# Optimization experiments

Measured on AMD Instinct MI355X. Metric: run time of the kernel, lower is better.

The kernel has to match this reference:

```python
import jax, jax.numpy as jnp
import numpy as np

D_MODEL = 1024
D_STATE = 128
D_CONV = 4
EXPAND = 2
HEADDIM = 64
D_INNER = EXPAND * D_MODEL            # 2048
NHEADS = D_INNER // HEADDIM           # 32
CONV_DIM = D_INNER + 2 * D_STATE      # 2304 (x, B, C share the conv)
D_IN_PROJ = 2 * D_INNER + 2 * D_STATE + NHEADS  # 4384 (z, xBC, dt)
CHUNK = 64
BATCH, SEQ = 8, 2048
EPS = 1e-5


def setup_inputs() -> dict:
    key = jax.random.key(0)
    ks = jax.random.split(key, 8)
    x = jax.random.normal(ks[0], (BATCH, SEQ, D_MODEL), dtype=jnp.float32)
    ln_w = jnp.ones((D_MODEL,), jnp.float32)
    ln_b = jnp.zeros((D_MODEL,), jnp.float32)
    W_in = jax.random.normal(ks[1], (D_IN_PROJ, D_MODEL), jnp.float32) * 0.02
    conv_w = jax.random.normal(ks[2], (CONV_DIM, D_CONV), jnp.float32) * 0.2
    conv_b = jnp.zeros((CONV_DIM,), jnp.float32)
    # dt_bias ~ inverse-softplus of dt in [1e-3, 1e-1]
    dt = jnp.exp(jax.random.uniform(ks[3], (NHEADS,), jnp.float32,
                                    minval=float(np.log(1e-3)), maxval=float(np.log(1e-1))))
    dt_bias = dt + jnp.log(-jnp.expm1(-dt))
    A_log = jnp.log(jax.random.uniform(ks[4], (NHEADS,), jnp.float32, minval=1.0, maxval=16.0))
    D = jnp.ones((NHEADS,), jnp.float32)
    rms_w = jnp.ones((D_INNER,), jnp.float32)
    W_out = jax.random.normal(ks[5], (D_MODEL, D_INNER), jnp.float32) * 0.02
    return {"x": x, "ln_w": ln_w, "ln_b": ln_b, "W_in": W_in, "conv_w": conv_w,
            "conv_b": conv_b, "dt_bias": dt_bias, "A_log": A_log, "D": D,
            "rms_w": rms_w, "W_out": W_out}


def _segsum(a):
    # a: (..., T) -> (..., T, T) cumulative segment sums, -inf above diagonal
    T = a.shape[-1]
    cs = jnp.cumsum(a, axis=-1)
    d = cs[..., :, None] - cs[..., None, :]
    return jnp.where(jnp.tril(jnp.ones((T, T), bool)), d, -jnp.inf)


def _mamba2_layer(x, ln_w, ln_b, W_in, conv_w, conv_b, dt_bias, A_log, D, rms_w, W_out):
    b, l, _ = x.shape
    # LayerNorm
    mu = jnp.mean(x, -1, keepdims=True)
    xc = x - mu
    var = jnp.mean(xc * xc, -1, keepdims=True)
    xn = xc * jax.lax.rsqrt(var + EPS) * ln_w + ln_b
    # in_proj -> z, xBC, dt
    zxbcdt = xn @ W_in.T                                  # (b,l,D_IN_PROJ)
    z = zxbcdt[..., :D_INNER]
    xBC = zxbcdt[..., D_INNER:D_INNER + CONV_DIM]
    dt = zxbcdt[..., D_INNER + CONV_DIM:]
    dt = jax.nn.softplus(dt + dt_bias)                    # (b,l,h)
    # causal depthwise conv1d (kernel D_CONV) + SiLU
    xp = jnp.pad(xBC, ((0, 0), (D_CONV - 1, 0), (0, 0)))
    conv = conv_b + sum(xp[:, k:k + l, :] * conv_w[:, k] for k in range(D_CONV))
    xBC = conv * jax.nn.sigmoid(conv)
    xs = xBC[..., :D_INNER].reshape(b, l, NHEADS, HEADDIM)          # (b,l,h,p)
    Bm = xBC[..., D_INNER:D_INNER + D_STATE]                         # (b,l,n) ngroups=1
    Cm = xBC[..., D_INNER + D_STATE:]                                # (b,l,n)
    # SSD chunked scan
    A = -jnp.exp(A_log)                                              # (h,)
    A_dt = dt * A                                                    # (b,l,h)
    Xdt = xs * dt[..., None]                                         # (b,l,h,p)
    nc = l // CHUNK
    Xc = Xdt.reshape(b, nc, CHUNK, NHEADS, HEADDIM)                  # (b,c,s,h,p)
    Ac = A_dt.reshape(b, nc, CHUNK, NHEADS).transpose(0, 3, 1, 2)    # (b,h,c,s)
    Bc = Bm.reshape(b, nc, CHUNK, D_STATE)                           # (b,c,s,n)
    Cc = Cm.reshape(b, nc, CHUNK, D_STATE)
    A_cs = jnp.cumsum(Ac, -1)                                        # (b,h,c,s)
    Lmat = jnp.exp(_segsum(Ac))                                      # (b,h,c,s,s)
    Y_diag = jnp.einsum('bcln,bcsn,bhcls,bcshp->bclhp', Cc, Bc, Lmat, Xc)
    decay_states = jnp.exp(A_cs[..., -1:] - A_cs)                    # (b,h,c,s)
    states = jnp.einsum('bcln,bhcl,bclhp->bchpn', Bc, decay_states, Xc)
    states = jnp.concatenate([jnp.zeros_like(states[:, :1]), states], axis=1)
    chunk_sum = jnp.pad(A_cs[..., -1], ((0, 0), (0, 0), (1, 0)))     # (b,h,c+1)
    decay_chunk = jnp.exp(_segsum(chunk_sum))                        # (b,h,c+1,c+1)
    new_states = jnp.einsum('bhzc,bchpn->bzhpn', decay_chunk, states)
    states_prev = new_states[:, :-1]                                 # (b,c,h,p,n)
    state_decay_out = jnp.exp(A_cs)                                  # (b,h,c,s)
    Y_off = jnp.einsum('bcln,bchpn,bhcl->bclhp', Cc, states_prev, state_decay_out)
    Y = (Y_diag + Y_off).reshape(b, l, NHEADS, HEADDIM)
    Y = Y + xs * D[None, None, :, None]
    y = Y.reshape(b, l, D_INNER)
    # gated RMSNorm: gate first, then normalize
    y = y * (z * jax.nn.sigmoid(z))
    y = y * jax.lax.rsqrt(jnp.mean(y * y, -1, keepdims=True) + EPS) * rms_w
    out = y @ W_out.T
    return x + out


def reference(x, ln_w, ln_b, W_in, conv_w, conv_b, dt_bias, A_log, D, rms_w, W_out):
    return _mamba2_layer(x, ln_w, ln_b, W_in, conv_w, conv_b, dt_bias, A_log, D, rms_w, W_out)
```

## Files before the change

### kernel.cpp

```cpp
#include <hip/hip_runtime.h>
#include <hip/hip_bf16.h>
#include <math.h>

typedef __hip_bfloat16 bf16;
typedef short short8 __attribute__((ext_vector_type(8)));
typedef short short4v __attribute__((ext_vector_type(4)));
typedef float f32x4 __attribute__((ext_vector_type(4)));

#define B_ 8
#define L_ 2048
#define DM 1024
#define DI 2048
#define NH 32
#define HD 64
#define DS 128
#define NWPAD 4480
#define XW 2432
#define CONVD 2304
#define NC 32
#define CK 64
#define HG 16
#define NGRP (NH / HG)
#define BL (B_ * L_)

static __device__ __forceinline__ f32x4 mfma_bf16(short8 a, short8 b, f32x4 c) {
  asm("v_mfma_f32_16x16x32_bf16 %0, %1, %2, %0" : "+v"(c) : "v"(a), "v"(b));
  return c;
}

static __device__ __forceinline__ void gload16(const bf16* g, bf16* l) {
  __builtin_amdgcn_global_load_lds((const __attribute__((address_space(1))) void*)g,
                                   (__attribute__((address_space(3))) void*)l, 16, 0, 0);
}

static __device__ __forceinline__ short bf2s(float f) {
  bf16 b = __float2bfloat16(f);
  return *reinterpret_cast<short*>(&b);
}

static __device__ __forceinline__ float s2f(short s) {
  unsigned int u = ((unsigned int)(unsigned short)s) << 16;
  return __uint_as_float(u);
}

__global__ void cvt_k(const float* __restrict__ Wi, const float* __restrict__ Wo,
                      bf16* __restrict__ Wib, bf16* __restrict__ Wob) {
  size_t i = (size_t)blockIdx.x * 256 + threadIdx.x;
  const size_t NWI = (size_t)NWPAD * DM;
  if (i < NWI) {
    float v = (i < (size_t)4384 * 1024) ? Wi[i] : 0.f;
    Wib[i] = __float2bfloat16(v);
  } else {
    size_t j = i - NWI;
    Wob[j] = __float2bfloat16(Wo[j]);
  }
}

__global__ void ln_k(const float* __restrict__ x, const float* __restrict__ w,
                     const float* __restrict__ bz, bf16* __restrict__ xn) {
  __shared__ float sm1[4], sm2[4];
  int row = blockIdx.x, tid = threadIdx.x;
  int d0 = tid * 4;
  const float* xr = x + (size_t)row * DM;
  float4 v4 = *(const float4*)&xr[d0];
  float v[4] = {v4.x, v4.y, v4.z, v4.w};
  float s = v[0] + v[1] + v[2] + v[3];
#pragma unroll
  for (int o = 32; o > 0; o >>= 1) s += __shfl_down(s, o, 64);
  if ((tid & 63) == 0) sm1[tid >> 6] = s;
  __syncthreads();
  float mean = (sm1[0] + sm1[1] + sm1[2] + sm1[3]) * (1.f / DM);
  float q = 0.f;
#pragma unroll
  for (int i = 0; i < 4; i++) { float d = v[i] - mean; q += d * d; }
#pragma unroll
  for (int o = 32; o > 0; o >>= 1) q += __shfl_down(q, o, 64);
  if ((tid & 63) == 0) sm2[tid >> 6] = q;
  __syncthreads();
  float rstd = rsqrtf((sm2[0] + sm2[1] + sm2[2] + sm2[3]) * (1.f / DM) + 1e-5f);
  float4 w4 = *(const float4*)&w[d0];
  float4 b4 = *(const float4*)&bz[d0];
  short4v o4;
  o4[0] = bf2s((v[0] - mean) * rstd * w4.x + b4.x);
  o4[1] = bf2s((v[1] - mean) * rstd * w4.y + b4.y);
  o4[2] = bf2s((v[2] - mean) * rstd * w4.z + b4.z);
  o4[3] = bf2s((v[3] - mean) * rstd * w4.w + b4.w);
  *(short4v*)&xn[(size_t)row * DM + d0] = o4;
}

#define GEMM_PROLOGUE(Kdim)                                                     \
  const int tid = threadIdx.x;                                                  \
  const int lane = tid & 63;                                                    \
  const int wave = tid >> 6;                                                    \
  int nwg = gridDim.x * gridDim.y;                                              \
  int id = blockIdx.y * gridDim.x + blockIdx.x;                                 \
  int bx = blockIdx.x, by = blockIdx.y;                                         \
  if ((nwg & 7) == 0) {                                                         \
    int swz = (id & 7) * (nwg >> 3) + (id >> 3);                                \
    bx = swz % gridDim.x;                                                       \
    by = swz / gridDim.x;                                                       \
  }                                                                             \
  const int m0 = by * 128, n0 = bx * 128;                                       \
  const int wm = (wave >> 1) * 64, wn = (wave & 1) * 64;                        \
  const int srow = tid >> 3;                                                    \
  const int schunk = tid & 7;                                                   \
  f32x4 acc[4][4];                                                              \
  _Pragma("unroll")                                                             \
  for (int i = 0; i < 4; i++)                                                   \
    _Pragma("unroll")                                                           \
    for (int j = 0; j < 4; j++) acc[i][j] = (f32x4){0.f, 0.f, 0.f, 0.f};        \
  for (int kt = 0; kt < (Kdim); kt += 64) {                                     \
    __syncthreads();                                                            \
    _Pragma("unroll")                                                           \
    for (int is = 0; is < 4; is++) {                                            \
      int row = is * 32 + srow;                                                 \
      int gcol = (schunk ^ (row & 7)) << 3;                                     \
      const bf16* ga = A + (size_t)(m0 + row) * (Kdim) + kt + gcol;             \
      const bf16* gb = Bw + (size_t)(n0 + row) * (Kdim) + kt + gcol;            \
      bf16* la = &As[(is * 32 + wave * 8) * 64];                                \
      bf16* lb = &Bs[(is * 32 + wave * 8) * 64];                                \
      gload16(ga, la);                                                          \
      gload16(gb, lb);                                                          \
    }                                                                           \
    __syncthreads();                                                            \
    _Pragma("unroll")                                                           \
    for (int kk = 0; kk < 2; kk++) {                                            \
      short8 af[4], bfr[4];                                                     \
      int mrow = lane & 15;                                                     \
      int kch = kk * 4 + (lane >> 4);                                           \
      _Pragma("unroll")                                                         \
      for (int mi = 0; mi < 4; mi++) {                                          \
        int r = wm + mi * 16 + mrow;                                            \
        af[mi] = *(const short8*)&As[r * 64 + ((kch ^ (r & 7)) << 3)];          \
      }                                                                         \
      _Pragma("unroll")                                                         \
      for (int ni = 0; ni < 4; ni++) {                                          \
        int r = wn + ni * 16 + mrow;                                            \
        bfr[ni] = *(const short8*)&Bs[r * 64 + ((kch ^ (r & 7)) << 3)];         \
      }                                                                         \
      _Pragma("unroll")                                                         \
      for (int mi = 0; mi < 4; mi++)                                            \
        _Pragma("unroll")                                                       \
        for (int ni = 0; ni < 4; ni++)                                          \
          acc[mi][ni] = mfma_bf16(af[mi], bfr[ni], acc[mi][ni]);                \
    }                                                                           \
  }                                                                             \
  asm volatile("s_nop 7\n\ts_nop 7" ::);                                        \
  const int orow = (lane >> 4) << 2;                                            \
  const int ocol = lane & 15;

__global__ __launch_bounds__(256) void gemm_inproj_k(
    const bf16* __restrict__ A, const bf16* __restrict__ Bw,
    bf16* __restrict__ zb, bf16* __restrict__ xb) {
  __shared__ bf16 As[128 * 64];
  __shared__ bf16 Bs[128 * 64];
  GEMM_PROLOGUE(DM)
#pragma unroll
  for (int mi = 0; mi < 4; mi++) {
#pragma unroll
    for (int ni = 0; ni < 4; ni++) {
      int rbase = m0 + wm + mi * 16 + orow;
      int cc = n0 + wn + ni * 16 + ocol;
#pragma unroll
      for (int r = 0; r < 4; r++) {
        bf16 v = __float2bfloat16(acc[mi][ni][r]);
        if (cc < DI) zb[(size_t)(rbase + r) * DI + cc] = v;
        else         xb[(size_t)(rbase + r) * XW + (cc - DI)] = v;
      }
    }
  }
}

__global__ __launch_bounds__(256) void gemm_out_k(
    const bf16* __restrict__ A, const bf16* __restrict__ Bw,
    float* __restrict__ C, const float* __restrict__ resid) {
  __shared__ bf16 As[128 * 64];
  __shared__ bf16 Bs[128 * 64];
  GEMM_PROLOGUE(DI)
#pragma unroll
  for (int mi = 0; mi < 4; mi++) {
#pragma unroll
    for (int ni = 0; ni < 4; ni++) {
      int rbase = m0 + wm + mi * 16 + orow;
      int cc = n0 + wn + ni * 16 + ocol;
#pragma unroll
      for (int r = 0; r < 4; r++) {
        size_t idx = (size_t)(rbase + r) * DM + cc;
        C[idx] = acc[mi][ni][r] + resid[idx];
      }
    }
  }
}

__global__ void conv_k(const bf16* __restrict__ xbc, const float* __restrict__ conv_w,
                       const float* __restrict__ conv_b, bf16* __restrict__ xsb,
                       bf16* __restrict__ Bb, bf16* __restrict__ Cb) {
  int c = blockIdx.x * 256 + threadIdx.x;
  int lbase = blockIdx.y * 16;
  int b = blockIdx.z;
  float4 w = ((const float4*)conv_w)[c];
  float bias = conv_b[c];
  const bf16* xp = xbc + (size_t)b * L_ * XW + c;
  float h0 = 0.f, h1 = 0.f, h2 = 0.f;
  if (lbase > 0) {
    h0 = __bfloat162float(xp[(size_t)(lbase - 3) * XW]);
    h1 = __bfloat162float(xp[(size_t)(lbase - 2) * XW]);
    h2 = __bfloat162float(xp[(size_t)(lbase - 1) * XW]);
  }
  for (int t = 0; t < 16; t++) {
    int l = lbase + t;
    float x3 = __bfloat162float(xp[(size_t)l * XW]);
    float v = bias + w.x * h0 + w.y * h1 + w.z * h2 + w.w * x3;
    v = v / (1.f + __expf(-v));
    bf16 o = __float2bfloat16(v);
    size_t rl = (size_t)b * L_ + l;
    if (c < DI)           xsb[rl * DI + c] = o;
    else if (c < DI + DS) Bb[rl * DS + (c - DI)] = o;
    else                  Cb[rl * DS + (c - DI - DS)] = o;
    h0 = h1; h1 = h2; h2 = x3;
  }
}

__global__ void dt_k(const bf16* __restrict__ xbc, const float* __restrict__ dt_bias,
                     const float* __restrict__ A_log, float* __restrict__ dtsp,
                     float* __restrict__ dta) {
  size_t i = (size_t)blockIdx.x * 256 + threadIdx.x;
  int h = (int)(i >> 14);
  size_t row = i & 16383;
  float raw = __bfloat162float(xbc[row * XW + CONVD + h]) + dt_bias[h];
  float sp = (raw > 20.f) ? raw : log1pf(__expf(raw));
  dtsp[i] = sp;
  dta[i] = -__expf(A_log[h]) * sp;
}

__global__ __launch_bounds__(256) void chunk_g_k(
    const bf16* __restrict__ xsb, const bf16* __restrict__ Bb, const bf16* __restrict__ Cb,
    const float* __restrict__ dtsp, const float* __restrict__ dta,
    const float* __restrict__ Dv, int hbase,
    bf16* __restrict__ Y, bf16* __restrict__ states, float* __restrict__ cs63) {
  __shared__ __align__(16) bf16 Bs[64][136];
  __shared__ __align__(16) bf16 Cs[64][136];
  __shared__ __align__(16) bf16 Btw[128][72];
  __shared__ __align__(16) bf16 Xt[64][72];
  __shared__ __align__(16) bf16 Sb[64][72];
  __shared__ float cs[64];
  __shared__ float wts[64];
  __shared__ float dts[64];

  int hgsub = blockIdx.x, c = blockIdx.y, b = blockIdx.z;
  int tid = threadIdx.x;
  int lane = tid & 63, wid = tid >> 6;
  size_t l0 = (size_t)b * L_ + (size_t)c * CK;

  for (int i = tid; i < 64 * 16; i += 256) {
    int r = i >> 4, n8 = (i & 15) << 3;
    *(short8*)&Bs[r][n8] = *(const short8*)&Bb[(l0 + r) * DS + n8];
    *(short8*)&Cs[r][n8] = *(const short8*)&Cb[(l0 + r) * DS + n8];
  }
  __syncthreads();

  f32x4 accg[4];
#pragma unroll
  for (int i = 0; i < 4; i++) accg[i] = (f32x4){0.f, 0.f, 0.f, 0.f};
  {
    int rb = wid * 16 + (lane & 15);
    int c0 = (lane >> 4) * 8;
#pragma unroll
    for (int kk = 0; kk < 4; kk++) {
      int kc = c0 + kk * 32;
      short8 bfrag = *(const short8*)&Bs[rb][kc];
#pragma unroll
      for (int lt = 0; lt < 4; lt++) {
        short8 afrag = *(const short8*)&Cs[lt * 16 + (lane & 15)][kc];
        accg[lt] = mfma_bf16(afrag, bfrag, accg[lt]);
      }
    }
  }
  asm volatile("s_nop 7\n\ts_nop 7" ::);

  for (int hh = 0; hh < 8; hh++) {
    int hl = hgsub * 8 + hh;
    int h = hbase + hl;
    __syncthreads();

    {
      const bf16* xp = xsb + l0 * DI + h * HD + lane;
      for (int oct = wid; oct < 8; oct += 4) {
        int lb = oct * 8;
        short8 v;
#pragma unroll
        for (int j = 0; j < 8; j++)
          v[j] = *(const short*)&xp[(size_t)(lb + j) * DI];
        *(short8*)&Xt[lane][lb] = v;
      }
    }
    if (tid < 64) {
      dts[tid] = dtsp[(size_t)h * BL + l0 + tid];
      wts[tid] = dta[(size_t)h * BL + l0 + tid];
    }
    __syncthreads();
    if (tid < 64) {
      float a = wts[tid];
#pragma unroll
      for (int o = 1; o < 64; o <<= 1) {
        float t = __shfl_up(a, o, 64);
        if (lane >= o) a += t;
      }
      cs[tid] = a;
      float tot = __shfl(a, 63, 64);
      if (tid == 63) cs63[((size_t)b * NH + h) * NC + c] = a;
      wts[tid] = __expf(tot - a) * dts[tid];
    }
    __syncthreads();

    for (int u = wid; u < 16; u += 4) {
      int nh = u & 1, oct = u >> 1;
      int n = nh * 64 + lane;
      int lb = oct * 8;
      short8 v;
#pragma unroll
      for (int j = 0; j < 8; j++)
        v[j] = bf2s(__bfloat162float(Bs[lb + j][n]) * wts[lb + j]);
      *(short8*)&Btw[n][lb] = v;
    }
    {
      int s = wid * 16 + (lane & 15);
      float css = cs[s], dtss = dts[s];
#pragma unroll
      for (int lt = 0; lt < 4; lt++) {
#pragma unroll
        for (int r = 0; r < 4; r++) {
          int l = lt * 16 + ((lane >> 4) << 2) + r;
          float v = (s <= l) ? accg[lt][r] * __expf(cs[l] - css) * dtss : 0.f;
          Sb[l][s] = __float2bfloat16(v);
        }
      }
    }
    __syncthreads();

    f32x4 accy[4];
#pragma unroll
    for (int i = 0; i < 4; i++) accy[i] = (f32x4){0.f, 0.f, 0.f, 0.f};
    {
      int prow = wid * 16 + (lane & 15);
      int c0 = (lane >> 4) * 8;
#pragma unroll
      for (int kk = 0; kk < 2; kk++) {
        int kc = c0 + kk * 32;
        short8 xfrag = *(const short8*)&Xt[prow][kc];
#pragma unroll
        for (int lt = 0; lt < 4; lt++) {
          short8 sfrag = *(const short8*)&Sb[lt * 16 + (lane & 15)][kc];
          accy[lt] = mfma_bf16(sfrag, xfrag, accy[lt]);
        }
      }
    }
    f32x4 accs[4][2];
#pragma unroll
    for (int i = 0; i < 4; i++)
#pragma unroll
      for (int j = 0; j < 2; j++) accs[i][j] = (f32x4){0.f, 0.f, 0.f, 0.f};
    {
      int c0 = (lane >> 4) * 8;
#pragma unroll
      for (int kk = 0; kk < 2; kk++) {
        int kc = c0 + kk * 32;
        short8 bf0 = *(const short8*)&Btw[wid * 32 + (lane & 15)][kc];
        short8 bf1 = *(const short8*)&Btw[wid * 32 + 16 + (lane & 15)][kc];
#pragma unroll
        for (int pt = 0; pt < 4; pt++) {
          short8 xfrag = *(const short8*)&Xt[pt * 16 + (lane & 15)][kc];
          accs[pt][0] = mfma_bf16(xfrag, bf0, accs[pt][0]);
          accs[pt][1] = mfma_bf16(xfrag, bf1, accs[pt][1]);
        }
      }
    }
    asm volatile("s_nop 7\n\ts_nop 7" ::);
    {
      float Dh = Dv[h];
      int p = wid * 16 + (lane & 15);
#pragma unroll
      for (int lt = 0; lt < 4; lt++) {
#pragma unroll
        for (int r = 0; r < 4; r++) {
          int l = lt * 16 + ((lane >> 4) << 2) + r;
          float xv = __bfloat162float(Xt[p][l]);
          Y[(l0 + l) * DI + h * HD + p] = __float2bfloat16(accy[lt][r] + Dh * xv);
        }
      }
    }
    {
      size_t sbb = ((((size_t)b * NC + c) * HG + hl) * HD) * DS;
#pragma unroll
      for (int pt = 0; pt < 4; pt++)
#pragma unroll
        for (int tn = 0; tn < 2; tn++)
#pragma unroll
          for (int r = 0; r < 4; r++) {
            int p = pt * 16 + ((lane >> 4) << 2) + r;
            int n = wid * 32 + tn * 16 + (lane & 15);
            states[sbb + (size_t)p * DS + n] = __float2bfloat16(accs[pt][tn][r]);
          }
    }
  }
}

__global__ void scan_k(bf16* __restrict__ states, const float* __restrict__ cs63,
                       int hbase) {
  int hl = blockIdx.x, b = blockIdx.y, sp = blockIdx.z;
  int tid = threadIdx.x;
  const float* csb = cs63 + ((size_t)b * NH + hbase + hl) * NC;
  int e0 = sp * 1024 + tid * 4;
  float S0 = 0.f, S1 = 0.f, S2 = 0.f, S3 = 0.f;
  for (int c = 0; c < NC; c++) {
    bf16* p = states + ((((size_t)b * NC + c) * HG + hl) * HD) * DS + e0;
    float d = __expf(csb[c]);
    short4v cur = *(const short4v*)p;
    short4v prev;
    prev[0] = bf2s(S0); prev[1] = bf2s(S1); prev[2] = bf2s(S2); prev[3] = bf2s(S3);
    *(short4v*)p = prev;
    S0 = S0 * d + s2f(cur[0]);
    S1 = S1 * d + s2f(cur[1]);
    S2 = S2 * d + s2f(cur[2]);
    S3 = S3 * d + s2f(cur[3]);
  }
}

__global__ __launch_bounds__(256) void yoff_k(
    const bf16* __restrict__ Cb, const bf16* __restrict__ states,
    const float* __restrict__ dta, int hbase, bf16* __restrict__ Y) {
  __shared__ __align__(16) bf16 Cs[64][136];
  __shared__ __align__(16) bf16 Sp[64][136];
  __shared__ float cs[64];
  int hl = blockIdx.x, c = blockIdx.y, b = blockIdx.z;
  int h = hbase + hl;
  int tid = threadIdx.x;
  int lane = tid & 63, wid = tid >> 6;
  size_t l0 = (size_t)b * L_ + (size_t)c * CK;
  for (int i = tid; i < 64 * 16; i += 256) {
    int r = i >> 4, n8 = (i & 15) << 3;
    *(short8*)&Cs[r][n8] = *(const short8*)&Cb[(l0 + r) * DS + n8];
  }
  size_t sbb = ((((size_t)b * NC + c) * HG + hl) * HD) * DS;
  for (int i = tid; i < 64 * 16; i += 256) {
    int p = i >> 4, n8 = (i & 15) << 3;
    *(short8*)&Sp[p][n8] = *(const short8*)&states[sbb + (size_t)p * DS + n8];
  }
  if (tid < 64) cs[tid] = dta[(size_t)h * BL + l0 + tid];
  __syncthreads();
  if (tid < 64) {
    float a = cs[tid];
#pragma unroll
    for (int o = 1; o < 64; o <<= 1) {
      float t = __shfl_up(a, o, 64);
      if (lane >= o) a += t;
    }
    cs[tid] = a;
  }
  __syncthreads();
  f32x4 acc[4];
#pragma unroll
  for (int i = 0; i < 4; i++) acc[i] = (f32x4){0.f, 0.f, 0.f, 0.f};
  {
    int prow = wid * 16 + (lane & 15);
    int c0 = (lane >> 4) * 8;
#pragma unroll
    for (int kk = 0; kk < 4; kk++) {
      int kc = c0 + kk * 32;
      short8 sfrag = *(const short8*)&Sp[prow][kc];
#pragma unroll
      for (int lt = 0; lt < 4; lt++) {
        short8 cfrag = *(const short8*)&Cs[lt * 16 + (lane & 15)][kc];
        acc[lt] = mfma_bf16(cfrag, sfrag, acc[lt]);
      }
    }
  }
  asm volatile("s_nop 7\n\ts_nop 7" ::);
  {
    int p = wid * 16 + (lane & 15);
#pragma unroll
    for (int lt = 0; lt < 4; lt++) {
#pragma unroll
      for (int r = 0; r < 4; r++) {
        int l = lt * 16 + ((lane >> 4) << 2) + r;
        float e = __expf(cs[l]);
        size_t idx = (l0 + l) * DI + h * HD + p;
        Y[idx] = __float2bfloat16(__bfloat162float(Y[idx]) + e * acc[lt][r]);
      }
    }
  }
}

__global__ void gate_k(const bf16* __restrict__ Y, const bf16* __restrict__ z,
                       const float* __restrict__ rms_w, bf16* __restrict__ yb) {
  __shared__ float sm[4];
  int row = blockIdx.x, tid = threadIdx.x;
  int d0 = tid * 8;
  const bf16* Yr = Y + (size_t)row * DI;
  const bf16* zr = z + (size_t)row * DI;
  short8 yv8 = *(const short8*)&Yr[d0];
  short8 zv8 = *(const short8*)&zr[d0];
  float v[8]; float ss = 0.f;
#pragma unroll
  for (int i = 0; i < 8; i++) {
    float yv = s2f(yv8[i]);
    float zz = s2f(zv8[i]);
    yv *= zz / (1.f + __expf(-zz));
    v[i] = yv; ss += yv * yv;
  }
#pragma unroll
  for (int o = 32; o > 0; o >>= 1) ss += __shfl_down(ss, o, 64);
  if ((tid & 63) == 0) sm[tid >> 6] = ss;
  __syncthreads();
  float rstd = rsqrtf((sm[0] + sm[1] + sm[2] + sm[3]) * (1.f / DI) + 1e-5f);
  short8 o8;
#pragma unroll
  for (int i = 0; i < 8; i++) o8[i] = bf2s(v[i] * rstd * rms_w[d0 + i]);
  *(short8*)&yb[(size_t)row * DI + d0] = o8;
}

extern "C" void kernel_launch(void* const* d_in, const int* in_sizes, int n_in,
                              void* d_out, int out_size, void* d_ws, size_t ws_size,
                              hipStream_t stream) {
  const float* x       = (const float*)d_in[0];
  const float* ln_w    = (const float*)d_in[1];
  const float* ln_b    = (const float*)d_in[2];
  const float* W_in    = (const float*)d_in[3];
  const float* conv_w  = (const float*)d_in[4];
  const float* conv_b  = (const float*)d_in[5];
  const float* dt_bias = (const float*)d_in[6];
  const float* A_log   = (const float*)d_in[7];
  const float* Dv      = (const float*)d_in[8];
  const float* rms_w   = (const float*)d_in[9];
  const float* W_out   = (const float*)d_in[10];
  float* out = (float*)d_out;

  char* ws = (char*)d_ws;
  size_t off = 0;
  auto alloc = [&](size_t bytes) -> void* {
    void* p = ws + off;
    off += (bytes + 255) & ~(size_t)255;
    return p;
  };
  bf16*  W_in_b  = (bf16*)alloc((size_t)NWPAD * DM * 2);
  bf16*  W_out_b = (bf16*)alloc((size_t)DM * DI * 2);
  bf16*  R1      = (bf16*)alloc((size_t)BL * XW * 2);
  bf16*  R2      = (bf16*)alloc((size_t)BL * DI * 2);
  bf16*  Bb      = (bf16*)alloc((size_t)BL * DS * 2);
  bf16*  Cb      = (bf16*)alloc((size_t)BL * DS * 2);
  float* dtsp    = (float*)alloc((size_t)BL * NH * 4);
  float* dta     = (float*)alloc((size_t)BL * NH * 4);
  float* cs63    = (float*)alloc((size_t)B_ * NH * NC * 4);
  bf16* xbcdt  = R1;
  bf16* states = R1;
  bf16* yb     = R1;
  bf16* xn     = R2;
  bf16* xsb    = R2;
  bf16* zbuf   = (bf16*)d_out;
  (void)ws_size; (void)in_sizes; (void)n_in; (void)out_size;

  cvt_k <<<(NWPAD * DM + DM * DI) / 256, 256, 0, stream>>>(W_in, W_out, W_in_b, W_out_b);
  ln_k  <<<BL, 256, 0, stream>>>(x, ln_w, ln_b, xn);
  gemm_inproj_k<<<dim3(NWPAD / 128, BL / 128), 256, 0, stream>>>(
      xn, W_in_b, zbuf, xbcdt);
  conv_k<<<dim3(CONVD / 256, L_ / 16, B_), 256, 0, stream>>>(
      xbcdt, conv_w, conv_b, xsb, Bb, Cb);
  dt_k  <<<(BL * NH) / 256, 256, 0, stream>>>(xbcdt, dt_bias, A_log, dtsp, dta);
  for (int g = 0; g < NGRP; g++) {
    int hbase = g * HG;
    chunk_g_k<<<dim3(2, NC, B_), 256, 0, stream>>>(xsb, Bb, Cb, dtsp, dta, Dv, hbase,
                                                   xsb , states, cs63);
    scan_k   <<<dim3(HG, B_, 8), 256, 0, stream>>>(states, cs63, hbase);
    yoff_k   <<<dim3(HG, NC, B_), 256, 0, stream>>>(Cb, states, dta, hbase, xsb );
  }
  gate_k<<<BL, 256, 0, stream>>>(xsb , zbuf, rms_w, yb);
  gemm_out_k<<<dim3(DM / 128, BL / 128), 256, 0, stream>>>(yb, W_out_b, out, x);
}
```

Baseline: 569.7 us.

## Rewrite GEMMs as 256x256 double-buffered pipelined tiles with 8 waves

```diff
diff --git a/kernel.cpp b/kernel.cpp
--- a/kernel.cpp
+++ b/kernel.cpp
@@ -14,7 +14,7 @@
 #define NH 32
 #define HD 64
 #define DS 128
-#define NWPAD 4480
+#define NWPAD 4608
 #define XW 2432
 #define CONVD 2304
 #define NC 32
@@ -88,7 +88,76 @@
   *(short4v*)&xn[(size_t)row * DM + d0] = o4;
 }
 
-#define GEMM_PROLOGUE(Kdim)                                                     \
+static __device__ __forceinline__ void stage_half(const bf16* __restrict__ gbase, int Kd,
+                                                  bf16* lbase, int H, int kti,
+                                                  int srow, int schunk, int wave) {
+  int gc = (schunk ^ (srow & 7)) << 3;
+  const bf16* g = gbase + (size_t)(H * 128 + srow) * Kd + (size_t)kti * 64 + gc;
+  bf16* l = lbase + (H * 128 + wave * 8) * 64;
+  gload16(g, l);
+  gload16(g + (size_t)64 * Kd, l + 64 * 64);
+}
+
+#define BARM asm volatile("s_barrier" ::: "memory")
+
+#define RD_A(mi)                                                                \
+  {                                                                             \
+    int r = wm + (mi) * 16 + (lane & 15);                                       \
+    int k0 = lane >> 4;                                                         \
+    af[mi][0] = *(const short8*)&Asb[r * 64 + ((k0 ^ (r & 7)) << 3)];           \
+    af[mi][1] = *(const short8*)&Asb[r * 64 + (((k0 + 4) ^ (r & 7)) << 3)];     \
+  }
+#define RD_B(ni)                                                                \
+  {                                                                             \
+    int r = wn + (ni) * 16 + (lane & 15);                                       \
+    int k0 = lane >> 4;                                                         \
+    bfr[ni][0] = *(const short8*)&Bsb[r * 64 + ((k0 ^ (r & 7)) << 3)];          \
+    bfr[ni][1] = *(const short8*)&Bsb[r * 64 + (((k0 + 4) ^ (r & 7)) << 3)];    \
+  }
+#define MFMA_Q(q)                                                               \
+  __builtin_amdgcn_s_setprio(1);                                                \
+  _Pragma("unroll") for (int ni = 0; ni < 4; ni++)                              \
+    acc[2*(q)][ni] = mfma_bf16(af[2*(q)][0], bfr[ni][0], acc[2*(q)][ni]);       \
+  _Pragma("unroll") for (int ni = 0; ni < 4; ni++)                              \
+    acc[2*(q)+1][ni] = mfma_bf16(af[2*(q)+1][0], bfr[ni][0], acc[2*(q)+1][ni]); \
+  _Pragma("unroll") for (int ni = 0; ni < 4; ni++)                              \
+    acc[2*(q)][ni] = mfma_bf16(af[2*(q)][1], bfr[ni][1], acc[2*(q)][ni]);       \
+  _Pragma("unroll") for (int ni = 0; ni < 4; ni++)                              \
+    acc[2*(q)+1][ni] = mfma_bf16(af[2*(q)+1][1], bfr[ni][1], acc[2*(q)+1][ni]); \
+  __builtin_amdgcn_s_setprio(0);
+
+#define TILE4(b, t, Kd)                                                         \
+  {                                                                             \
+    const bf16* Asb = &As[b][0];                                                \
+    const bf16* Bsb = &Bs[b][0];                                                \
+    const int i1 = ((t) + 1 < NKT) ? (t) + 1 : NKT - 1;                         \
+    const int i2 = ((t) + 2 < NKT) ? (t) + 2 : NKT - 1;                         \
+    RD_B(0) RD_B(1) RD_B(2) RD_B(3)                                             \
+    RD_A(0) RD_A(1)                                                             \
+    stage_half(Ag, Kd, &As[(b) ^ 1][0], 1, i1, srow, schunk, wave);             \
+    asm volatile("s_waitcnt lgkmcnt(8)" ::: "memory");                          \
+    BARM;                                                                       \
+    MFMA_Q(0)                                                                   \
+    BARM;                                                                       \
+    RD_A(2) RD_A(3) RD_A(4) RD_A(5)                                             \
+    stage_half(Bg, Kd, &Bs[b][0], 0, i2, srow, schunk, wave);                   \
+    BARM;                                                                       \
+    MFMA_Q(1)                                                                   \
+    BARM;                                                                       \
+    RD_A(6) RD_A(7)                                                             \
+    stage_half(Bg, Kd, &Bs[b][0], 1, i2, srow, schunk, wave);                   \
+    asm volatile("s_waitcnt lgkmcnt(0)" ::: "memory");                          \
+    BARM;                                                                       \
+    MFMA_Q(2)                                                                   \
+    BARM;                                                                       \
+    stage_half(Ag, Kd, &As[b][0], 0, i2, srow, schunk, wave);                   \
+    asm volatile("s_waitcnt vmcnt(6)" ::: "memory");                            \
+    BARM;                                                                       \
+    MFMA_Q(3)                                                                   \
+    BARM;                                                                       \
+  }
+
+#define GEMM8_BODY(Kd)                                                          \
   const int tid = threadIdx.x;                                                  \
   const int lane = tid & 63;                                                    \
   const int wave = tid >> 6;                                                    \
@@ -100,63 +169,44 @@
     bx = swz % gridDim.x;                                                       \
     by = swz / gridDim.x;                                                       \
   }                                                                             \
-  const int m0 = by * 128, n0 = bx * 128;                                       \
-  const int wm = (wave >> 1) * 64, wn = (wave & 1) * 64;                        \
-  const int srow = tid >> 3;                                                    \
-  const int schunk = tid & 7;                                                   \
-  f32x4 acc[4][4];                                                              \
-  _Pragma("unroll")                                                             \
-  for (int i = 0; i < 4; i++)                                                   \
-    _Pragma("unroll")                                                           \
-    for (int j = 0; j < 4; j++) acc[i][j] = (f32x4){0.f, 0.f, 0.f, 0.f};        \
-  for (int kt = 0; kt < (Kdim); kt += 64) {                                     \
-    __syncthreads();                                                            \
-    _Pragma("unroll")                                                           \
-    for (int is = 0; is < 4; is++) {                                            \
-      int row = is * 32 + srow;                                                 \
-      int gcol = (schunk ^ (row & 7)) << 3;                                     \
-      const bf16* ga = A + (size_t)(m0 + row) * (Kdim) + kt + gcol;             \
-      const bf16* gb = Bw + (size_t)(n0 + row) * (Kdim) + kt + gcol;            \
-      bf16* la = &As[(is * 32 + wave * 8) * 64];                                \
-      bf16* lb = &Bs[(is * 32 + wave * 8) * 64];                                \
-      gload16(ga, la);                                                          \
-      gload16(gb, lb);                                                          \
-    }                                                                           \
-    __syncthreads();                                                            \
-    _Pragma("unroll")                                                           \
-    for (int kk = 0; kk < 2; kk++) {                                            \
-      short8 af[4], bfr[4];                                                     \
-      int mrow = lane & 15;                                                     \
-      int kch = kk * 4 + (lane >> 4);                                           \
-      _Pragma("unroll")                                                         \
-      for (int mi = 0; mi < 4; mi++) {                                          \
-        int r = wm + mi * 16 + mrow;                                            \
-        af[mi] = *(const short8*)&As[r * 64 + ((kch ^ (r & 7)) << 3)];          \
-      }                                                                         \
-      _Pragma("unroll")                                                         \
-      for (int ni = 0; ni < 4; ni++) {                                          \
-        int r = wn + ni * 16 + mrow;                                            \
-        bfr[ni] = *(const short8*)&Bs[r * 64 + ((kch ^ (r & 7)) << 3)];         \
-      }                                                                         \
-      _Pragma("unroll")                                                         \
-      for (int mi = 0; mi < 4; mi++)                                            \
-        _Pragma("unroll")                                                       \
-        for (int ni = 0; ni < 4; ni++)                                          \
-          acc[mi][ni] = mfma_bf16(af[mi], bfr[ni], acc[mi][ni]);                \
-    }                                                                           \
+  const int m0 = by * 256, n0 = bx * 256;                                       \
+  const int wm = (wave >> 2) * 128, wn = (wave & 3) * 64;                       \
+  const int srow = tid >> 3, schunk = tid & 7;                                  \
+  const bf16* Ag = A + (size_t)m0 * (Kd);                                       \
+  const bf16* Bg = Bw + (size_t)n0 * (Kd);                                      \
+  const int NKT = (Kd) / 64;                                                    \
+  f32x4 acc[8][4];                                                              \
+  short8 af[8][2], bfr[4][2];                                                   \
+  _Pragma("unroll") for (int i = 0; i < 8; i++)                                 \
+    _Pragma("unroll") for (int j = 0; j < 4; j++)                               \
+      acc[i][j] = (f32x4){0.f, 0.f, 0.f, 0.f};                                  \
+  stage_half(Bg, Kd, &Bs[0][0], 0, 0, srow, schunk, wave);                      \
+  stage_half(Bg, Kd, &Bs[0][0], 1, 0, srow, schunk, wave);                      \
+  stage_half(Ag, Kd, &As[0][0], 0, 0, srow, schunk, wave);                      \
+  stage_half(Ag, Kd, &As[0][0], 1, 0, srow, schunk, wave);                      \
+  asm volatile("s_waitcnt vmcnt(4)" ::: "memory");                              \
+  stage_half(Bg, Kd, &Bs[1][0], 0, 1, srow, schunk, wave);                      \
+  stage_half(Bg, Kd, &Bs[1][0], 1, 1, srow, schunk, wave);                      \
+  stage_half(Ag, Kd, &As[1][0], 0, 1, srow, schunk, wave);                      \
+  asm volatile("s_waitcnt vmcnt(6)" ::: "memory");                              \
+  BARM;                                                                         \
+  for (int t = 0; t < NKT; t += 2) {                                            \
+    TILE4(0, t, Kd)                                                             \
+    TILE4(1, t + 1, Kd)                                                         \
   }                                                                             \
+  asm volatile("s_waitcnt vmcnt(0)" ::: "memory");                              \
   asm volatile("s_nop 7\n\ts_nop 7" ::);                                        \
   const int orow = (lane >> 4) << 2;                                            \
   const int ocol = lane & 15;
 
-__global__ __launch_bounds__(256) void gemm_inproj_k(
+__global__ __launch_bounds__(512, 2) void gemm_inproj_k(
     const bf16* __restrict__ A, const bf16* __restrict__ Bw,
     bf16* __restrict__ zb, bf16* __restrict__ xb) {
-  __shared__ bf16 As[128 * 64];
-  __shared__ bf16 Bs[128 * 64];
-  GEMM_PROLOGUE(DM)
-#pragma unroll
-  for (int mi = 0; mi < 4; mi++) {
+  __shared__ bf16 As[2][256 * 64];
+  __shared__ bf16 Bs[2][256 * 64];
+  GEMM8_BODY(DM)
+#pragma unroll
+  for (int mi = 0; mi < 8; mi++) {
 #pragma unroll
     for (int ni = 0; ni < 4; ni++) {
       int rbase = m0 + wm + mi * 16 + orow;
@@ -164,21 +214,21 @@
 #pragma unroll
       for (int r = 0; r < 4; r++) {
         bf16 v = __float2bfloat16(acc[mi][ni][r]);
-        if (cc < DI) zb[(size_t)(rbase + r) * DI + cc] = v;
-        else         xb[(size_t)(rbase + r) * XW + (cc - DI)] = v;
-      }
-    }
-  }
-}
-
-__global__ __launch_bounds__(256) void gemm_out_k(
+        if (cc < DI)               zb[(size_t)(rbase + r) * DI + cc] = v;
+        else if (cc < DI + XW)     xb[(size_t)(rbase + r) * XW + (cc - DI)] = v;
+      }
+    }
+  }
+}
+
+__global__ __launch_bounds__(512, 2) void gemm_out_k(
     const bf16* __restrict__ A, const bf16* __restrict__ Bw,
     float* __restrict__ C, const float* __restrict__ resid) {
-  __shared__ bf16 As[128 * 64];
-  __shared__ bf16 Bs[128 * 64];
-  GEMM_PROLOGUE(DI)
-#pragma unroll
-  for (int mi = 0; mi < 4; mi++) {
+  __shared__ bf16 As[2][256 * 64];
+  __shared__ bf16 Bs[2][256 * 64];
+  GEMM8_BODY(DI)
+#pragma unroll
+  for (int mi = 0; mi < 8; mi++) {
 #pragma unroll
     for (int ni = 0; ni < 4; ni++) {
       int rbase = m0 + wm + mi * 16 + orow;
@@ -561,7 +611,7 @@
 
   cvt_k <<<(NWPAD * DM + DM * DI) / 256, 256, 0, stream>>>(W_in, W_out, W_in_b, W_out_b);
   ln_k  <<<BL, 256, 0, stream>>>(x, ln_w, ln_b, xn);
-  gemm_inproj_k<<<dim3(NWPAD / 128, BL / 128), 256, 0, stream>>>(
+  gemm_inproj_k<<<dim3(NWPAD / 256, BL / 256), 512, 0, stream>>>(
       xn, W_in_b, zbuf, xbcdt);
   conv_k<<<dim3(CONVD / 256, L_ / 16, B_), 256, 0, stream>>>(
       xbcdt, conv_w, conv_b, xsb, Bb, Cb);
@@ -574,5 +624,5 @@
     yoff_k   <<<dim3(HG, NC, B_), 256, 0, stream>>>(Cb, states, dta, hbase, xsb );
   }
   gate_k<<<BL, 256, 0, stream>>>(xsb , zbuf, rms_w, yb);
-  gemm_out_k<<<dim3(DM / 128, BL / 128), 256, 0, stream>>>(yb, W_out_b, out, x);
-}
+  gemm_out_k<<<dim3(DM / 256, BL / 256), 512, 0, stream>>>(yb, W_out_b, out, x);
+}
```

Measured after the change: 567.7 us. About the same (-0.4%).
